# Kernel optimization log

Measured on AMD Instinct MI355X. Metric: run time of the kernel, lower is better.

The kernel has to match this reference:

```python
import jax, jax.numpy as jnp
import numpy as np

B, C, H, W = 256, 32, 64, 64


def _affine_grid(theta, Hs, Ws):
    # theta: [B,2,3]; align_corners=False (PyTorch default). Returns [B,H,W,2] with (x,y) order.
    xs = (2.0 * jnp.arange(Ws, dtype=theta.dtype) + 1.0) / Ws - 1.0  # [W]
    ys = (2.0 * jnp.arange(Hs, dtype=theta.dtype) + 1.0) / Hs - 1.0  # [H]
    Xg, Yg = jnp.meshgrid(xs, ys)                                    # [H,W] each
    base = jnp.stack([Xg, Yg, jnp.ones_like(Xg)], axis=-1)           # [H,W,3]
    return jnp.einsum('bij,hwj->bhwi', theta, base)                  # [B,H,W,2]


def _grid_sample_bilinear(x, grid):
    # x: [B,C,H,W]; grid: [B,H,W,2] normalized (x,y); bilinear, zero padding, align_corners=False.
    Bs, Cs, Hs, Ws = x.shape
    gx = (grid[..., 0] + 1.0) * (Ws * 0.5) - 0.5
    gy = (grid[..., 1] + 1.0) * (Hs * 0.5) - 0.5
    x0 = jnp.floor(gx); y0 = jnp.floor(gy)
    x1 = x0 + 1.0;      y1 = y0 + 1.0
    wx1 = gx - x0; wx0 = 1.0 - wx1
    wy1 = gy - y0; wy0 = 1.0 - wy1

    def corner(xf, yf, w):
        valid = (xf >= 0) & (xf <= Ws - 1) & (yf >= 0) & (yf <= Hs - 1)
        xi = jnp.clip(xf, 0, Ws - 1).astype(jnp.int32)
        yi = jnp.clip(yf, 0, Hs - 1).astype(jnp.int32)
        vals = jax.vmap(lambda img, yy, xx: img[:, yy, xx])(x, yi, xi)  # [B,C,H,W] gather
        return vals * (w * valid)[:, None, :, :]

    return (corner(x0, y0, wx0 * wy0) + corner(x1, y0, wx1 * wy0)
            + corner(x0, y1, wx0 * wy1) + corner(x1, y1, wx1 * wy1))


def reference(x, w1, b1, w2, b2, w3, b3):
    Bs = x.shape[0]
    xs = x.reshape(Bs, -1)
    xs = jax.nn.relu(xs @ w1.T + b1)
    xs = jax.nn.relu(xs @ w2.T + b2)
    theta = (xs @ w3.T + b3).reshape(Bs, 2, 3)
    grid = _affine_grid(theta, x.shape[2], x.shape[3])
    return _grid_sample_bilinear(x, grid)


def setup_inputs() -> dict:
    key = jax.random.key(0)
    ks = jax.random.split(key, 8)
    fan1 = C * H * W
    x = jax.random.normal(ks[0], (B, C, H, W), dtype=jnp.float32)
    w1 = jax.random.normal(ks[1], (32, fan1), dtype=jnp.float32) / np.sqrt(fan1)
    b1 = jax.random.normal(ks[2], (32,), dtype=jnp.float32) * 0.01
    w2 = jax.random.normal(ks[3], (32, 32), dtype=jnp.float32) / np.sqrt(32.0)
    b2 = jax.random.normal(ks[4], (32,), dtype=jnp.float32) * 0.01
    w3 = jax.random.normal(ks[5], (6, 32), dtype=jnp.float32) * 0.001
    identity = jnp.array([1.0, 0.0, 0.0, 0.0, 1.0, 0.0], dtype=jnp.float32)
    b3 = identity + jax.random.normal(ks[6], (6,), dtype=jnp.float32) * 0.01
    return {"x": x, "w1": w1, "b1": b1, "w2": w2, "b2": b2, "w3": w3, "b3": b3}
```

## Files before the change

### kernel.cpp

```cpp
#include <hip/hip_runtime.h>
#include <hip/hip_bf16.h>
#include <hip/hip_cooperative_groups.h>

namespace cg = cooperative_groups;


#define K_TOT 131072
#define KC    256
#define PKN   1024
#define STRB  ((size_t)PKN * 32)

typedef short s16x8 __attribute__((ext_vector_type(8)));
typedef float f32x4 __attribute__((ext_vector_type(4)));

__device__ __forceinline__ short f2bf(float f) {
    return __builtin_bit_cast(short, __float2bfloat16(f));
}

__device__ __forceinline__ s16x8 cvt8(float4 a, float4 b) {
    s16x8 r;
    r[0] = f2bf(a.x); r[1] = f2bf(a.y); r[2] = f2bf(a.z); r[3] = f2bf(a.w);
    r[4] = f2bf(b.x); r[5] = f2bf(b.y); r[6] = f2bf(b.z); r[7] = f2bf(b.w);
    return r;
}

__device__ __forceinline__ void gload_lds16(const float* g, float* l) {
    __builtin_amdgcn_global_load_lds(
        (const __attribute__((address_space(1))) void*)(g),
        (__attribute__((address_space(3))) void*)(l),
        16, 0, 0);
}

__device__ __forceinline__ void phase1(int bid, const float* __restrict__ x,
                                       const float* __restrict__ w1,
                                       float* __restrict__ partial, char* smem) {
    float* xbuf = (float*)smem;
    s16x8* wlds = (s16x8*)(smem + 16384);

    const int t    = threadIdx.x;
    const int wv   = t >> 6;
    const int lane = t & 63;
    const int m    = lane & 15;
    const int kb   = lane >> 4;
    const int jh   = wv & 1;
    const int kh   = wv >> 1;

    const int xcd  = bid & 7;
    const int q    = bid >> 3;
    const int kc   = xcd * 64 + (q >> 1);
    const int half = q & 1;
    const size_t k0 = (size_t)kc * KC;

#pragma unroll
    for (int i = 0; i < 4; ++i) {
        const int f  = i * 256 + t;
        const int fm = f & 15, fk = (f >> 4) & 3, fj = (f >> 6) & 1, fs = f >> 7;
        const float* wp = w1 + (size_t)(fj * 16 + fm) * K_TOT + k0 + fs * 32 + fk * 8;
        wlds[f] = cvt8(*(const float4*)wp, *(const float4*)(wp + 4));
    }

    const int pk = kc * 2 + kh;
    for (int it = 0; it < 8; ++it) {
        const int b0 = half * 128 + it * 16;
        __syncthreads();
#pragma unroll
        for (int i2 = 0; i2 < 4; ++i2) {
            const int r = wv * 4 + i2;
            const float* gsrc = x + (size_t)(b0 + r) * K_TOT + k0 + ((lane ^ (r & 7)) << 2);
            gload_lds16(gsrc, xbuf + r * 256);
        }
        __syncthreads();

        const float* xr = xbuf + m * 256;
        const int sw = m & 7;
        f32x4 acc = {0.f, 0.f, 0.f, 0.f};
#pragma unroll
        for (int sss = 0; sss < 4; ++sss) {
            const int gb = kh * 32 + sss * 8 + kb * 2;
            const float4 fa = *(const float4*)(xr + ((gb ^ sw) << 2));
            const float4 fb = *(const float4*)(xr + (((gb + 1) ^ sw) << 2));
            const s16x8 af = cvt8(fa, fb);
            const s16x8 bf = wlds[((kh * 4 + sss) * 2 + jh) * 64 + lane];
            acc = __builtin_amdgcn_mfma_f32_16x16x32_bf16(af, bf, acc, 0, 0, 0);
        }
        float* p0 = partial + (size_t)(b0 + kb * 4) * STRB + (size_t)pk * 32 + jh * 16 + m;
#pragma unroll
        for (int rr = 0; rr < 4; ++rr)
            p0[(size_t)rr * STRB] = acc[rr];
    }
}

__device__ __forceinline__ void phase2(int b, const float* __restrict__ partial,
                                       const float* __restrict__ b1,
                                       const float* __restrict__ w2,
                                       const float* __restrict__ b2,
                                       const float* __restrict__ w3,
                                       const float* __restrict__ b3,
                                       float* __restrict__ theta, char* smem) {
    const int t = threadIdx.x;
    const float* pb = partial + (size_t)b * STRB;

    float4 v = {0.f, 0.f, 0.f, 0.f};
#pragma unroll
    for (int i = 0; i < 32; ++i) {
        const float4 u = *(const float4*)(pb + (size_t)(i * 256 + t) * 4);
        v.x += u.x; v.y += u.y; v.z += u.z; v.w += u.w;
    }

    float4* red = (float4*)smem;
    float*  s1s = (float*)(smem + 4096);
    float*  s2s = (float*)(smem + 4224);
    red[t] = v;
    __syncthreads();
#pragma unroll
    for (int off = 128; off >= 8; off >>= 1) {
        if (t < off) {
            float4 a = red[t];
            const float4 c = red[t + off];
            a.x += c.x; a.y += c.y; a.z += c.z; a.w += c.w;
            red[t] = a;
        }
        __syncthreads();
    }
    if (t < 8) {
        const float4 qd = red[t];
        s1s[4 * t + 0] = fmaxf(qd.x + b1[4 * t + 0], 0.f);
        s1s[4 * t + 1] = fmaxf(qd.y + b1[4 * t + 1], 0.f);
        s1s[4 * t + 2] = fmaxf(qd.z + b1[4 * t + 2], 0.f);
        s1s[4 * t + 3] = fmaxf(qd.w + b1[4 * t + 3], 0.f);
    }
    __syncthreads();
    if (t < 32) {
        float vv = b2[t];
#pragma unroll
        for (int i = 0; i < 32; ++i) vv += w2[t * 32 + i] * s1s[i];
        s2s[t] = fmaxf(vv, 0.f);
    }
    __syncthreads();
    if (t < 8) {
        float vv = 0.f;
        if (t < 6) {
            vv = b3[t];
#pragma unroll
            for (int i = 0; i < 32; ++i) vv += w3[t * 32 + i] * s2s[i];
        }
        theta[b * 8 + t] = vv;
    }
}

__device__ __forceinline__ void phase3(int bid, const float* __restrict__ x,
                                       const float* __restrict__ theta,
                                       float* __restrict__ out) {
    const int b  = bid >> 2;
    const int h0 = (bid & 3) * 16;
    const int t  = threadIdx.x;
    const int w  = t & 63;
    const int c0 = t >> 6;

    const float* tb = theta + b * 8;
    const float t0 = tb[0], t1 = tb[1], t2 = tb[2];
    const float t3 = tb[3], t4 = tb[4], t5 = tb[5];

    for (int r = 0; r < 16; ++r) {
        const int h = h0 + r;
        const float xs = ((float)w - 31.5f) * 0.03125f;
        const float ys = ((float)h - 31.5f) * 0.03125f;
        const float gxn = fmaf(t1, ys, fmaf(t0, xs, t2));
        const float gyn = fmaf(t4, ys, fmaf(t3, xs, t5));
        const float gx = fmaf(gxn, 32.f, 31.5f);
        const float gy = fmaf(gyn, 32.f, 31.5f);
        const float x0f = floorf(gx), y0f = floorf(gy);
        const float wx1 = gx - x0f, wx0 = 1.f - wx1;
        const float wy1 = gy - y0f, wy0 = 1.f - wy1;
        const int ix = (int)x0f, iy = (int)y0f;
        const bool vx0 = (ix >= 0) && (ix < 64);
        const bool vx1 = (ix >= -1) && (ix < 63);
        const bool vy0 = (iy >= 0) && (iy < 64);
        const bool vy1 = (iy >= -1) && (iy < 63);
        const int cx0 = min(max(ix, 0), 63);
        const int cx1 = min(max(ix + 1, 0), 63);
        const int cy0 = min(max(iy, 0), 63);
        const int cy1 = min(max(iy + 1, 0), 63);
        const float w00 = wx0 * wy0 * ((vx0 && vy0) ? 1.f : 0.f);
        const float w10 = wx1 * wy0 * ((vx1 && vy0) ? 1.f : 0.f);
        const float w01 = wx0 * wy1 * ((vx0 && vy1) ? 1.f : 0.f);
        const float w11 = wx1 * wy1 * ((vx1 && vy1) ? 1.f : 0.f);
        const int r0 = cy0 * 64, r1 = cy1 * 64;
#pragma unroll
        for (int i = 0; i < 8; ++i) {
            const int c = c0 + 4 * i;
            const float* img = x + (((size_t)b * 32 + c) << 12);
            const float v = w00 * img[r0 + cx0] + w10 * img[r0 + cx1]
                          + w01 * img[r1 + cx0] + w11 * img[r1 + cx1];
            __builtin_nontemporal_store(v, &out[(((size_t)b * 32 + c) << 12) + h * 64 + w]);
        }
    }
}

__global__ __launch_bounds__(256, 4) void st_coop(const float* __restrict__ x,
                                                  const float* __restrict__ w1,
                                                  const float* __restrict__ b1,
                                                  const float* __restrict__ w2,
                                                  const float* __restrict__ b2,
                                                  const float* __restrict__ w3,
                                                  const float* __restrict__ b3,
                                                  float* __restrict__ out,
                                                  float* __restrict__ ws) {
    cg::grid_group grid = cg::this_grid();
    __shared__ __align__(16) char smem[32768];
    float* partial = ws;
    float* theta   = ws + (size_t)256 * STRB;

    phase1(blockIdx.x, x, w1, partial, smem);
    grid.sync();
    if (blockIdx.x < 256)
        phase2(blockIdx.x, partial, b1, w2, b2, w3, b3, theta, smem);
    grid.sync();
    phase3(blockIdx.x, x, theta, out);
}

__global__ __launch_bounds__(256) void st_p1k(const float* __restrict__ x,
                                              const float* __restrict__ w1,
                                              float* __restrict__ partial) {
    __shared__ __align__(16) char smem[32768];
    phase1(blockIdx.x, x, w1, partial, smem);
}

__global__ __launch_bounds__(256) void st_p2k(const float* __restrict__ partial,
                                              const float* __restrict__ b1,
                                              const float* __restrict__ w2,
                                              const float* __restrict__ b2,
                                              const float* __restrict__ w3,
                                              const float* __restrict__ b3,
                                              float* __restrict__ theta) {
    __shared__ __align__(16) char smem[4352];
    phase2(blockIdx.x, partial, b1, w2, b2, w3, b3, theta, smem);
}

__global__ __launch_bounds__(256) void st_p3k(const float* __restrict__ x,
                                              const float* __restrict__ theta,
                                              float* __restrict__ out) {
    phase3(blockIdx.x, x, theta, out);
}

extern "C" void kernel_launch(void* const* d_in, const int* in_sizes, int n_in,
                              void* d_out, int out_size, void* d_ws, size_t ws_size,
                              hipStream_t stream) {
    const float* x  = (const float*)d_in[0];
    const float* w1 = (const float*)d_in[1];
    const float* b1 = (const float*)d_in[2];
    const float* w2 = (const float*)d_in[3];
    const float* b2 = (const float*)d_in[4];
    const float* w3 = (const float*)d_in[5];
    const float* b3 = (const float*)d_in[6];
    float* out = (float*)d_out;
    float* ws  = (float*)d_ws;
    float* partial = ws;
    float* theta   = ws + (size_t)256 * STRB;

    bool launched = false;
    if (ws_size >= ((size_t)256 * STRB + 2048) * sizeof(float)) {
        int ncu = 0, nblk = 0, dev = 0;
        (void)hipGetDevice(&dev);
        (void)hipDeviceGetAttribute(&ncu, hipDeviceAttributeMultiprocessorCount, dev);
        (void)hipOccupancyMaxActiveBlocksPerMultiprocessor(&nblk, st_coop, 256, 0);
        if (ncu > 0 && nblk > 0 && (long long)nblk * ncu >= 1024) {
            void* args[] = {(void*)&x, (void*)&w1, (void*)&b1, (void*)&w2, (void*)&b2,
                            (void*)&w3, (void*)&b3, (void*)&out, (void*)&ws};
            launched = (hipLaunchCooperativeKernel((void*)st_coop, dim3(1024), dim3(256),
                                                   args, 0, stream) == hipSuccess);
        }
    }
    if (!launched) {
        st_p1k<<<1024, 256, 0, stream>>>(x, w1, partial);
        st_p2k<<<256, 256, 0, stream>>>(partial, b1, w2, b2, w3, b3, theta);
        st_p3k<<<1024, 256, 0, stream>>>(x, theta, out);
    }
}
```

Baseline: 88.19 us.

## Replace cooperative grid-sync kernel with three launches and double-buffer phase-one loads

Removes the cooperative single-kernel path with two grid-wide syncs and always launches three separate kernels. The first stage now double-buffers its x tiles in LDS: the next tile's async global-to-LDS load is issued before the MFMA work on the current tile, with one barrier per iteration instead of two. The sampling stage is split into 2048 blocks of 8 rows each instead of 1024 blocks of 16 rows. In exchange it pays extra launch gaps between stages and more LDS per block (48 KB), which can lower occupancy for the first stage.

Result: no change. 88.33 us (+0.2%).

```diff
diff --git a/kernel.cpp b/kernel.cpp
--- a/kernel.cpp
+++ b/kernel.cpp
@@ -1,8 +1,5 @@
 #include <hip/hip_runtime.h>
 #include <hip/hip_bf16.h>
-#include <hip/hip_cooperative_groups.h>
-
-namespace cg = cooperative_groups;
 
 
 #define K_TOT 131072
@@ -31,12 +28,15 @@
         16, 0, 0);
 }
 
-__device__ __forceinline__ void phase1(int bid, const float* __restrict__ x,
-                                       const float* __restrict__ w1,
-                                       float* __restrict__ partial, char* smem) {
-    float* xbuf = (float*)smem;
-    s16x8* wlds = (s16x8*)(smem + 16384);
-
+__global__ __launch_bounds__(256) void st_p1k(const float* __restrict__ x,
+                                              const float* __restrict__ w1,
+                                              float* __restrict__ partial) {
+    __shared__ __align__(16) char smem[49152];
+    float* xbuf0 = (float*)smem;
+    float* xbuf1 = (float*)(smem + 16384);
+    s16x8* wlds  = (s16x8*)(smem + 32768);
+
+    const int bid  = blockIdx.x;
     const int t    = threadIdx.x;
     const int wv   = t >> 6;
     const int lane = t & 63;
@@ -51,6 +51,15 @@
     const int half = q & 1;
     const size_t k0 = (size_t)kc * KC;
 
+    {
+        const int b0 = half * 128;
+#pragma unroll
+        for (int i2 = 0; i2 < 4; ++i2) {
+            const int r = wv * 4 + i2;
+            const float* gsrc = x + (size_t)(b0 + r) * K_TOT + k0 + ((lane ^ (r & 7)) << 2);
+            gload_lds16(gsrc, xbuf0 + r * 256);
+        }
+    }
 #pragma unroll
     for (int i = 0; i < 4; ++i) {
         const int f  = i * 256 + t;
@@ -60,19 +69,24 @@
     }
 
     const int pk = kc * 2 + kh;
+    const int sw = m & 7;
+#pragma unroll
     for (int it = 0; it < 8; ++it) {
-        const int b0 = half * 128 + it * 16;
         __syncthreads();
-#pragma unroll
-        for (int i2 = 0; i2 < 4; ++i2) {
-            const int r = wv * 4 + i2;
-            const float* gsrc = x + (size_t)(b0 + r) * K_TOT + k0 + ((lane ^ (r & 7)) << 2);
-            gload_lds16(gsrc, xbuf + r * 256);
-        }
-        __syncthreads();
-
-        const float* xr = xbuf + m * 256;
-        const int sw = m & 7;
+
+        if (it < 7) {
+            float* nbuf = ((it + 1) & 1) ? xbuf1 : xbuf0;
+            const int b0n = half * 128 + (it + 1) * 16;
+#pragma unroll
+            for (int i2 = 0; i2 < 4; ++i2) {
+                const int r = wv * 4 + i2;
+                const float* gsrc = x + (size_t)(b0n + r) * K_TOT + k0 + ((lane ^ (r & 7)) << 2);
+                gload_lds16(gsrc, nbuf + r * 256);
+            }
+        }
+
+        const float* cbuf = (it & 1) ? xbuf1 : xbuf0;
+        const float* xr = cbuf + m * 256;
         f32x4 acc = {0.f, 0.f, 0.f, 0.f};
 #pragma unroll
         for (int sss = 0; sss < 4; ++sss) {
@@ -83,6 +97,7 @@
             const s16x8 bf = wlds[((kh * 4 + sss) * 2 + jh) * 64 + lane];
             acc = __builtin_amdgcn_mfma_f32_16x16x32_bf16(af, bf, acc, 0, 0, 0);
         }
+        const int b0 = half * 128 + it * 16;
         float* p0 = partial + (size_t)(b0 + kb * 4) * STRB + (size_t)pk * 32 + jh * 16 + m;
 #pragma unroll
         for (int rr = 0; rr < 4; ++rr)
@@ -90,13 +105,14 @@
     }
 }
 
-__device__ __forceinline__ void phase2(int b, const float* __restrict__ partial,
-                                       const float* __restrict__ b1,
-                                       const float* __restrict__ w2,
-                                       const float* __restrict__ b2,
-                                       const float* __restrict__ w3,
-                                       const float* __restrict__ b3,
-                                       float* __restrict__ theta, char* smem) {
+__global__ __launch_bounds__(256) void st_p2k(const float* __restrict__ partial,
+                                              const float* __restrict__ b1,
+                                              const float* __restrict__ w2,
+                                              const float* __restrict__ b2,
+                                              const float* __restrict__ w3,
+                                              const float* __restrict__ b3,
+                                              float* __restrict__ theta) {
+    const int b = blockIdx.x;
     const int t = threadIdx.x;
     const float* pb = partial + (size_t)b * STRB;
 
@@ -107,9 +123,9 @@
         v.x += u.x; v.y += u.y; v.z += u.z; v.w += u.w;
     }
 
-    float4* red = (float4*)smem;
-    float*  s1s = (float*)(smem + 4096);
-    float*  s2s = (float*)(smem + 4224);
+    __shared__ float4 red[256];
+    __shared__ float s1s[32];
+    __shared__ float s2s[32];
     red[t] = v;
     __syncthreads();
 #pragma unroll
@@ -148,20 +164,21 @@
     }
 }
 
-__device__ __forceinline__ void phase3(int bid, const float* __restrict__ x,
-                                       const float* __restrict__ theta,
-                                       float* __restrict__ out) {
-    const int b  = bid >> 2;
-    const int h0 = (bid & 3) * 16;
-    const int t  = threadIdx.x;
-    const int w  = t & 63;
-    const int c0 = t >> 6;
+__global__ __launch_bounds__(256) void st_p3k(const float* __restrict__ x,
+                                              const float* __restrict__ theta,
+                                              float* __restrict__ out) {
+    const int bid = blockIdx.x;
+    const int b   = bid >> 3;
+    const int h0  = (bid & 7) * 8;
+    const int t   = threadIdx.x;
+    const int w   = t & 63;
+    const int c0  = t >> 6;
 
     const float* tb = theta + b * 8;
     const float t0 = tb[0], t1 = tb[1], t2 = tb[2];
     const float t3 = tb[3], t4 = tb[4], t5 = tb[5];
 
-    for (int r = 0; r < 16; ++r) {
+    for (int r = 0; r < 8; ++r) {
         const int h = h0 + r;
         const float xs = ((float)w - 31.5f) * 0.03125f;
         const float ys = ((float)h - 31.5f) * 0.03125f;
@@ -197,52 +214,6 @@
     }
 }
 
-__global__ __launch_bounds__(256, 4) void st_coop(const float* __restrict__ x,
-                                                  const float* __restrict__ w1,
-                                                  const float* __restrict__ b1,
-                                                  const float* __restrict__ w2,
-                                                  const float* __restrict__ b2,
-                                                  const float* __restrict__ w3,
-                                                  const float* __restrict__ b3,
-                                                  float* __restrict__ out,
-                                                  float* __restrict__ ws) {
-    cg::grid_group grid = cg::this_grid();
-    __shared__ __align__(16) char smem[32768];
-    float* partial = ws;
-    float* theta   = ws + (size_t)256 * STRB;
-
-    phase1(blockIdx.x, x, w1, partial, smem);
-    grid.sync();
-    if (blockIdx.x < 256)
-        phase2(blockIdx.x, partial, b1, w2, b2, w3, b3, theta, smem);
-    grid.sync();
-    phase3(blockIdx.x, x, theta, out);
-}
-
-__global__ __launch_bounds__(256) void st_p1k(const float* __restrict__ x,
-                                              const float* __restrict__ w1,
-                                              float* __restrict__ partial) {
-    __shared__ __align__(16) char smem[32768];
-    phase1(blockIdx.x, x, w1, partial, smem);
-}
-
-__global__ __launch_bounds__(256) void st_p2k(const float* __restrict__ partial,
-                                              const float* __restrict__ b1,
-                                              const float* __restrict__ w2,
-                                              const float* __restrict__ b2,
-                                              const float* __restrict__ w3,
-                                              const float* __restrict__ b3,
-                                              float* __restrict__ theta) {
-    __shared__ __align__(16) char smem[4352];
-    phase2(blockIdx.x, partial, b1, w2, b2, w3, b3, theta, smem);
-}
-
-__global__ __launch_bounds__(256) void st_p3k(const float* __restrict__ x,
-                                              const float* __restrict__ theta,
-                                              float* __restrict__ out) {
-    phase3(blockIdx.x, x, theta, out);
-}
-
 extern "C" void kernel_launch(void* const* d_in, const int* in_sizes, int n_in,
                               void* d_out, int out_size, void* d_ws, size_t ws_size,
                               hipStream_t stream) {
@@ -258,22 +229,7 @@
     float* partial = ws;
     float* theta   = ws + (size_t)256 * STRB;
 
-    bool launched = false;
-    if (ws_size >= ((size_t)256 * STRB + 2048) * sizeof(float)) {
-        int ncu = 0, nblk = 0, dev = 0;
-        (void)hipGetDevice(&dev);
-        (void)hipDeviceGetAttribute(&ncu, hipDeviceAttributeMultiprocessorCount, dev);
-        (void)hipOccupancyMaxActiveBlocksPerMultiprocessor(&nblk, st_coop, 256, 0);
-        if (ncu > 0 && nblk > 0 && (long long)nblk * ncu >= 1024) {
-            void* args[] = {(void*)&x, (void*)&w1, (void*)&b1, (void*)&w2, (void*)&b2,
-                            (void*)&w3, (void*)&b3, (void*)&out, (void*)&ws};
-            launched = (hipLaunchCooperativeKernel((void*)st_coop, dim3(1024), dim3(256),
-                                                   args, 0, stream) == hipSuccess);
-        }
-    }
-    if (!launched) {
-        st_p1k<<<1024, 256, 0, stream>>>(x, w1, partial);
-        st_p2k<<<256, 256, 0, stream>>>(partial, b1, w2, b2, w3, b3, theta);
-        st_p3k<<<1024, 256, 0, stream>>>(x, theta, out);
-    }
-}
+    st_p1k<<<1024, 256, 0, stream>>>(x, w1, partial);
+    st_p2k<<<256, 256, 0, stream>>>(partial, b1, w2, b2, w3, b3, theta);
+    st_p3k<<<2048, 256, 0, stream>>>(x, theta, out);
+}
```
